# Kernel tuning notes

Hardware: AMD Instinct MI355X
Metric: run time of the kernel (lower is better)

## Reference

```python
import jax, jax.numpy as jnp
import numpy as np

EMBED_DIM = 512
NUM_HEADS = 8
HEAD_DIM = EMBED_DIM // NUM_HEADS
SCALE = HEAD_DIM ** -0.5


def setup_inputs() -> dict:
    key = jax.random.key(0)
    ks = jax.random.split(key, 5)
    B, N, C = 4, 2048, EMBED_DIM
    s = 0.02
    return {
        "x": jax.random.normal(ks[0], (B, N, C), jnp.float32),
        "qkv_w": jax.random.normal(ks[1], (3 * C, C), jnp.float32) * s,
        "qkv_b": jax.random.normal(ks[2], (3 * C,), jnp.float32) * s,
        "proj_w": jax.random.normal(ks[3], (C, C), jnp.float32) * s,
        "proj_b": jax.random.normal(ks[4], (C,), jnp.float32) * s,
    }


def reference(x, qkv_w, qkv_b, proj_w, proj_b):
    B, N, C = x.shape
    H, D = NUM_HEADS, HEAD_DIM
    # qkv: (B, N, 3C) -> (3, B, H, N, D)
    qkv = x @ qkv_w.T + qkv_b
    qkv = qkv.reshape(B, N, 3, H, D).transpose(2, 0, 3, 1, 4)
    q, k, v = qkv[0], qkv[1], qkv[2]
    attn = jnp.einsum("bhnd,bhmd->bhnm", q, k) * SCALE  # (B,H,N,N)
    attn = jax.nn.softmax(attn, axis=-1)
    out = jnp.einsum("bhnm,bhmd->bhnd", attn, v)  # (B,H,N,D)
    out = out.transpose(0, 2, 1, 3).reshape(B, N, C)
    return out @ proj_w.T + proj_b
```

## Files before the change

### kernel.cpp

```cpp
#include <hip/hip_runtime.h>

#define ED 512
#define NH 8
#define HD 64
#define BB 4
#define SEQ 2048
#define MTOT (BB*SEQ)

typedef float f32x4 __attribute__((ext_vector_type(4)));
typedef float f32x16 __attribute__((ext_vector_type(16)));
typedef __bf16 bf16x8 __attribute__((ext_vector_type(8)));
typedef int i32x2 __attribute__((ext_vector_type(2)));
typedef unsigned int u32x4 __attribute__((ext_vector_type(4)));

__device__ __forceinline__ unsigned short f2bf(float f) {
  unsigned int u = __float_as_uint(f);
  u += 0x7FFFu + ((u >> 16) & 1u);
  return (unsigned short)(u >> 16);
}

__device__ __forceinline__ unsigned int cvtpk(float lo, float hi) {
  unsigned int r;
  asm volatile("v_cvt_pk_bf16_f32 %0, %1, %2" : "=v"(r) : "v"(lo), "v"(hi));
  return r;
}

__device__ __forceinline__ void async16(const void* g, void* l) {
  auto gp = (const __attribute__((address_space(1))) unsigned int*)(uintptr_t)(g);
  auto lp = (__attribute__((address_space(3))) unsigned int*)(uintptr_t)(l);
  __builtin_amdgcn_global_load_lds(gp, lp, 16, 0, 0);
}

#define N4_X   1048576
#define N4_WQ  196608
#define N4_WP  65536
__global__ void cvt_all(const float* __restrict__ x,
                        const float* __restrict__ wq_in,
                        const float* __restrict__ wp_in,
                        unsigned short* __restrict__ xb,
                        unsigned short* __restrict__ wq,
                        unsigned short* __restrict__ wp) {
  int i = blockIdx.x * blockDim.x + threadIdx.x;
  const float* src; unsigned short* dst; int off;
  if (i < N4_X)              { src = x;     dst = xb; off = i; }
  else if (i < N4_X + N4_WQ) { src = wq_in; dst = wq; off = i - N4_X; }
  else                       { src = wp_in; dst = wp; off = i - (N4_X + N4_WQ); }
  float4 v = reinterpret_cast<const float4*>(src)[off];
  ushort4 o;
  o.x = f2bf(v.x); o.y = f2bf(v.y); o.z = f2bf(v.z); o.w = f2bf(v.w);
  reinterpret_cast<ushort4*>(dst)[off] = o;
}

template<int MODE, int BM>
__global__ __launch_bounds__(256)
void gemm_bt(const unsigned short* __restrict__ A,
             const unsigned short* __restrict__ B,
             const float* __restrict__ bias,
             int M, int N, int K,
             unsigned short* __restrict__ Qo,
             unsigned short* __restrict__ Ko,
             unsigned short* __restrict__ Vo,
             float* __restrict__ Co) {
  __shared__ __align__(16) unsigned short As[2][BM * 64];
  __shared__ __align__(16) unsigned short Bs[2][128 * 64];
  const int FI = BM / 32;
  const int t = threadIdx.x;
  const int l = t & 63;
  const int w = t >> 6;
  const int lo = l & 15, hi = l >> 4;
  const int wr = w >> 1, wc = w & 1;
  const int m0 = blockIdx.y * BM;
  const int n0 = blockIdx.x * 128;

  f32x4 acc[FI][4] = {};

  auto stage = [&](int buf, int kt) {
    #pragma unroll
    for (int it = 0; it < BM / 32; ++it) {
      int c = it * 256 + t;
      int row = c >> 3, cin = c & 7;
      int sw = cin ^ (row & 7);
      async16(A + (size_t)(m0 + row) * K + kt * 64 + sw * 8, &As[buf][c * 8]);
    }
    #pragma unroll
    for (int it = 0; it < 4; ++it) {
      int c = it * 256 + t;
      int row = c >> 3, cin = c & 7;
      int sw = cin ^ (row & 7);
      async16(B + (size_t)(n0 + row) * K + kt * 64 + sw * 8, &Bs[buf][c * 8]);
    }
  };

  const int nkt = K >> 6;
  stage(0, 0);
  asm volatile("s_waitcnt vmcnt(0)" ::: "memory");
  __syncthreads();

  for (int kt = 0; kt < nkt; ++kt) {
    const int cur = kt & 1;
    if (kt + 1 < nkt) stage(cur ^ 1, kt + 1);

    __builtin_amdgcn_s_setprio(1);
    #pragma unroll
    for (int kk = 0; kk < 2; ++kk) {
      bf16x8 af[FI], bf[4];
      #pragma unroll
      for (int i = 0; i < FI; ++i) {
        int ra = wr * (BM / 2) + i * 16 + lo;
        int ch = (kk * 4 + hi) ^ (lo & 7);
        af[i] = *reinterpret_cast<const bf16x8*>(&As[cur][ra * 64 + ch * 8]);
      }
      #pragma unroll
      for (int j = 0; j < 4; ++j) {
        int rb = wc * 64 + j * 16 + lo;
        int ch = (kk * 4 + hi) ^ (lo & 7);
        bf[j] = *reinterpret_cast<const bf16x8*>(&Bs[cur][rb * 64 + ch * 8]);
      }
      #pragma unroll
      for (int i = 0; i < FI; ++i)
        #pragma unroll
        for (int j = 0; j < 4; ++j)
          acc[i][j] = __builtin_amdgcn_mfma_f32_16x16x32_bf16(af[i], bf[j], acc[i][j], 0, 0, 0);
    }
    __builtin_amdgcn_s_setprio(0);

    asm volatile("s_waitcnt vmcnt(0)" ::: "memory");
    __syncthreads();
  }

  if (MODE == 0) {
    #pragma unroll
    for (int j = 0; j < 4; ++j) {
      int gcol = n0 + wc * 64 + j * 16 + lo;
      float bv = bias[gcol];
      int which = gcol >> 9;
      int h = (gcol >> 6) & 7;
      int d = gcol & 63;
      #pragma unroll
      for (int i = 0; i < FI; ++i) {
        int rbase = m0 + wr * (BM / 2) + i * 16 + hi * 4;
        int b = rbase >> 11;
        size_t bh = (size_t)(b * NH + h);
        if (which == 2) {
          ushort4 pk;
          pk.x = f2bf(acc[i][j][0] + bv);
          pk.y = f2bf(acc[i][j][1] + bv);
          pk.z = f2bf(acc[i][j][2] + bv);
          pk.w = f2bf(acc[i][j][3] + bv);
          int seq = rbase & 2047;
          *reinterpret_cast<ushort4*>(&Vo[(bh * HD + d) * SEQ + seq]) = pk;
        } else {
          #pragma unroll
          for (int e = 0; e < 4; ++e) {
            int seq = (rbase + e) & 2047;
            float v = acc[i][j][e] + bv;
            if (which == 0)
              Qo[(bh * SEQ + seq) * HD + d] = f2bf(v * 0.18033688f);
            else
              Ko[(bh * SEQ + seq) * HD + d] = f2bf(v);
          }
        }
      }
    }
  } else {
    #pragma unroll
    for (int j = 0; j < 4; ++j) {
      int gcol = n0 + wc * 64 + j * 16 + lo;
      float bv = bias[gcol];
      #pragma unroll
      for (int i = 0; i < FI; ++i) {
        int rbase = m0 + wr * (BM / 2) + i * 16 + hi * 4;
        #pragma unroll
        for (int e = 0; e < 4; ++e)
          Co[(size_t)(rbase + e) * N + gcol] = acc[i][j][e] + bv;
      }
    }
  }
}

__global__ __launch_bounds__(512, 4)
void attn_kernel(const unsigned short* __restrict__ Q,
                 const unsigned short* __restrict__ Kk,
                 const unsigned short* __restrict__ Vt,
                 unsigned short* __restrict__ Ao) {
  __shared__ __align__(16) unsigned short Ks[2][2][64 * 64];
  __shared__ __align__(16) unsigned short Vs[2][2][64 * 64];
  const int t = threadIdx.x;
  const int l = t & 63;
  const int wid = t >> 6;
  const int qg = wid & 3;
  const int kvh = wid >> 2;
  const int l31 = l & 31, lh = l >> 5;
  const int bh = blockIdx.y;
  const int q0 = blockIdx.x * 128;
  const int b = bh >> 3, h = bh & 7;

  bf16x8 qf[4];
  #pragma unroll
  for (int ks = 0; ks < 4; ++ks)
    qf[ks] = *reinterpret_cast<const bf16x8*>(
        &Q[((size_t)bh * SEQ + q0 + qg * 32 + l31) * HD + ks * 16 + lh * 8]);

  f32x16 o0 = {}, o1 = {}, osum = {};
  const __bf16 one1 = (__bf16)1.0f;
  const bf16x8 ones = {one1, one1, one1, one1, one1, one1, one1, one1};

  auto stage = [&](int buf, int kt) {
    const int half = t >> 8;
    const int tt = t & 255;
    const int sbase = half * 1024 + kt * 64;
    #pragma unroll
    for (int it = 0; it < 2; ++it) {
      int c = it * 256 + tt;
      int row = c >> 3, cin = c & 7;
      int sw = cin ^ (row & 7);
      async16(&Kk[((size_t)bh * SEQ + sbase + row) * HD + sw * 8],
              &Ks[half][buf][c * 8]);
    }
    #pragma unroll
    for (int it = 0; it < 2; ++it) {
      int c = it * 256 + tt;
      int row = c >> 3, cin = c & 7;
      int sw = cin ^ (row & 7);
      async16(&Vt[((size_t)bh * HD + row) * SEQ + sbase + sw * 8],
              &Vs[half][buf][c * 8]);
    }
  };

  auto tile = [&](int cur, int kt) {
    if (kt + 1 < 16) stage(cur ^ 1, kt + 1);

    #pragma unroll
    for (int kn = 0; kn < 2; ++kn) {
      f32x16 s = {};
      __builtin_amdgcn_s_setprio(1);
      #pragma unroll
      for (int ks = 0; ks < 4; ++ks) {
        int row = kn * 32 + l31;
        int ch = ((ks * 2 + lh) ^ (l31 & 7)) * 8;
        bf16x8 kf = *reinterpret_cast<const bf16x8*>(&Ks[kvh][cur][row * 64 + ch]);
        s = __builtin_amdgcn_mfma_f32_32x32x16_bf16(kf, qf[ks], s, 0, 0, 0);
      }
      __builtin_amdgcn_s_setprio(0);

      #pragma unroll
      for (int i = 0; i < 16; ++i) s[i] = __builtin_amdgcn_exp2f(s[i]);

      #pragma unroll
      for (int hs = 0; hs < 2; ++hs) {
        unsigned int w0 = cvtpk(s[8 * hs + 0], s[8 * hs + 1]);
        unsigned int w1 = cvtpk(s[8 * hs + 2], s[8 * hs + 3]);
        unsigned int w2 = cvtpk(s[8 * hs + 4], s[8 * hs + 5]);
        unsigned int w3 = cvtpk(s[8 * hs + 6], s[8 * hs + 7]);
        i32x2 r0 = __builtin_amdgcn_permlane32_swap((int)w0, (int)w2, false, false);
        i32x2 r1 = __builtin_amdgcn_permlane32_swap((int)w1, (int)w3, false, false);
        u32x4 fw = {(unsigned int)r0.x, (unsigned int)r1.x,
                    (unsigned int)r0.y, (unsigned int)r1.y};
        bf16x8 pf = __builtin_bit_cast(bf16x8, fw);

        int ss = kn * 2 + hs;
        int vch = ((ss * 2 + lh) ^ (l31 & 7)) * 8;
        __builtin_amdgcn_s_setprio(1);
        osum = __builtin_amdgcn_mfma_f32_32x32x16_bf16(pf, ones, osum, 0, 0, 0);
        bf16x8 vf0 = *reinterpret_cast<const bf16x8*>(&Vs[kvh][cur][l31 * 64 + vch]);
        bf16x8 vf1 = *reinterpret_cast<const bf16x8*>(&Vs[kvh][cur][(32 + l31) * 64 + vch]);
        o0 = __builtin_amdgcn_mfma_f32_32x32x16_bf16(pf, vf0, o0, 0, 0, 0);
        o1 = __builtin_amdgcn_mfma_f32_32x32x16_bf16(pf, vf1, o1, 0, 0, 0);
        __builtin_amdgcn_s_setprio(0);
      }
    }

    asm volatile("s_waitcnt vmcnt(0)" ::: "memory");
    __syncthreads();
  };

  stage(0, 0);
  asm volatile("s_waitcnt vmcnt(0)" ::: "memory");
  __syncthreads();

  for (int k2 = 0; k2 < 8; ++k2) {
    tile(0, 2 * k2);
    tile(1, 2 * k2 + 1);
  }

  float* lds = reinterpret_cast<float*>(&Ks[0][0][0]);
  if (kvh == 1) {
    int base = (qg * 64 + l) * 48;
    *reinterpret_cast<f32x16*>(&lds[base])      = o0;
    *reinterpret_cast<f32x16*>(&lds[base + 16]) = o1;
    *reinterpret_cast<f32x16*>(&lds[base + 32]) = osum;
  }
  __syncthreads();
  if (kvh == 0) {
    int base = (qg * 64 + l) * 48;
    o0   += *reinterpret_cast<const f32x16*>(&lds[base]);
    o1   += *reinterpret_cast<const f32x16*>(&lds[base + 16]);
    osum += *reinterpret_cast<const f32x16*>(&lds[base + 32]);

    #pragma unroll
    for (int r = 0; r < 16; ++r) {
      int qoff = (r & 3) + 8 * (r >> 2) + 4 * lh;
      int seq = q0 + qg * 32 + qoff;
      float inv = 1.f / osum[r];
      size_t base2 = ((size_t)b * SEQ + seq) * ED + h * HD;
      Ao[base2 + l31]      = f2bf(o0[r] * inv);
      Ao[base2 + 32 + l31] = f2bf(o1[r] * inv);
    }
  }
}

extern "C" void kernel_launch(void* const* d_in, const int* in_sizes, int n_in,
                              void* d_out, int out_size, void* d_ws, size_t ws_size,
                              hipStream_t stream) {
  const float* x      = (const float*)d_in[0];
  const float* qkv_w  = (const float*)d_in[1];
  const float* qkv_b  = (const float*)d_in[2];
  const float* proj_w = (const float*)d_in[3];
  const float* proj_b = (const float*)d_in[4];
  float* out = (float*)d_out;

  char* ws = (char*)d_ws;
  unsigned short* xb = (unsigned short*)(ws);
  unsigned short* wq = (unsigned short*)(ws + 8388608);
  unsigned short* wp = (unsigned short*)(ws + 9961472);
  unsigned short* Q  = (unsigned short*)(ws + 10485760);
  unsigned short* Kb = (unsigned short*)(ws + 18874368);
  unsigned short* Vt = (unsigned short*)(ws + 27262976);
  unsigned short* Ao = (unsigned short*)(ws + 35651584);

  cvt_all<<<(N4_X + N4_WQ + N4_WP + 255) / 256, 256, 0, stream>>>(
      x, qkv_w, proj_w, xb, wq, wp);

  dim3 g1(12, 128);
  gemm_bt<0, 64><<<g1, 256, 0, stream>>>(xb, wq, qkv_b, MTOT, 3 * ED, ED, Q, Kb, Vt, nullptr);

  dim3 ga(SEQ / 128, BB * NH);
  attn_kernel<<<ga, 512, 0, stream>>>(Q, Kb, Vt, Ao);

  dim3 g2(4, 128);
  gemm_bt<1, 64><<<g2, 256, 0, stream>>>(Ao, wp, proj_b, MTOT, ED, ED, nullptr, nullptr, nullptr, out);
}
```

Measured before the change: 86.88 us.

## Halve attention waves, give each wave two query sub-tiles to reuse K/V fragments

The attention kernel now launches 256 threads per block instead of 512. Each wave processes two 32-row query sub-tiles, so every K and V fragment read from LDS feeds two MFMAs, which halves LDS read traffic per unit of compute. The final cross-KV-half reduction uses a swizzled float4 LDS layout split across the K and V buffers. In exchange, register pressure roughly doubles (six accumulators plus two sets of Q fragments), fewer waves are available to hide latency, and each thread issues twice as many async copies when staging tiles.

```diff
diff --git a/kernel.cpp b/kernel.cpp
--- a/kernel.cpp
+++ b/kernel.cpp
@@ -178,7 +178,7 @@
   }
 }
 
-__global__ __launch_bounds__(512, 4)
+__global__ __launch_bounds__(256, 2)
 void attn_kernel(const unsigned short* __restrict__ Q,
                  const unsigned short* __restrict__ Kk,
                  const unsigned short* __restrict__ Vt,
@@ -188,38 +188,41 @@
   const int t = threadIdx.x;
   const int l = t & 63;
   const int wid = t >> 6;
-  const int qg = wid & 3;
-  const int kvh = wid >> 2;
+  const int qg = wid >> 1;
+  const int kvh = wid & 1;
   const int l31 = l & 31, lh = l >> 5;
   const int bh = blockIdx.y;
   const int q0 = blockIdx.x * 128;
   const int b = bh >> 3, h = bh & 7;
 
-  bf16x8 qf[4];
+  bf16x8 qfA[4], qfB[4];
   #pragma unroll
-  for (int ks = 0; ks < 4; ++ks)
-    qf[ks] = *reinterpret_cast<const bf16x8*>(
-        &Q[((size_t)bh * SEQ + q0 + qg * 32 + l31) * HD + ks * 16 + lh * 8]);
-
-  f32x16 o0 = {}, o1 = {}, osum = {};
+  for (int ks = 0; ks < 4; ++ks) {
+    size_t rowA = (size_t)bh * SEQ + q0 + qg * 64 + l31;
+    qfA[ks] = *reinterpret_cast<const bf16x8*>(&Q[rowA * HD + ks * 16 + lh * 8]);
+    qfB[ks] = *reinterpret_cast<const bf16x8*>(&Q[(rowA + 32) * HD + ks * 16 + lh * 8]);
+  }
+
+  f32x16 oA0 = {}, oA1 = {}, osA = {};
+  f32x16 oB0 = {}, oB1 = {}, osB = {};
   const __bf16 one1 = (__bf16)1.0f;
   const bf16x8 ones = {one1, one1, one1, one1, one1, one1, one1, one1};
 
   auto stage = [&](int buf, int kt) {
-    const int half = t >> 8;
-    const int tt = t & 255;
+    const int half = t >> 7;
+    const int tt = t & 127;
     const int sbase = half * 1024 + kt * 64;
     #pragma unroll
-    for (int it = 0; it < 2; ++it) {
-      int c = it * 256 + tt;
+    for (int it = 0; it < 4; ++it) {
+      int c = it * 128 + tt;
       int row = c >> 3, cin = c & 7;
       int sw = cin ^ (row & 7);
       async16(&Kk[((size_t)bh * SEQ + sbase + row) * HD + sw * 8],
               &Ks[half][buf][c * 8]);
     }
     #pragma unroll
-    for (int it = 0; it < 2; ++it) {
-      int c = it * 256 + tt;
+    for (int it = 0; it < 4; ++it) {
+      int c = it * 128 + tt;
       int row = c >> 3, cin = c & 7;
       int sw = cin ^ (row & 7);
       async16(&Vt[((size_t)bh * HD + row) * SEQ + sbase + sw * 8],
@@ -227,45 +230,57 @@
     }
   };
 
+  auto pack = [&](const f32x16& s, int hs) -> bf16x8 {
+    unsigned int w0 = cvtpk(s[8 * hs + 0], s[8 * hs + 1]);
+    unsigned int w1 = cvtpk(s[8 * hs + 2], s[8 * hs + 3]);
+    unsigned int w2 = cvtpk(s[8 * hs + 4], s[8 * hs + 5]);
+    unsigned int w3 = cvtpk(s[8 * hs + 6], s[8 * hs + 7]);
+    i32x2 r0 = __builtin_amdgcn_permlane32_swap((int)w0, (int)w2, false, false);
+    i32x2 r1 = __builtin_amdgcn_permlane32_swap((int)w1, (int)w3, false, false);
+    u32x4 fw = {(unsigned int)r0.x, (unsigned int)r1.x,
+                (unsigned int)r0.y, (unsigned int)r1.y};
+    return __builtin_bit_cast(bf16x8, fw);
+  };
+
   auto tile = [&](int cur, int kt) {
     if (kt + 1 < 16) stage(cur ^ 1, kt + 1);
 
     #pragma unroll
     for (int kn = 0; kn < 2; ++kn) {
-      f32x16 s = {};
+      f32x16 s0 = {}, s1 = {};
       __builtin_amdgcn_s_setprio(1);
       #pragma unroll
       for (int ks = 0; ks < 4; ++ks) {
         int row = kn * 32 + l31;
         int ch = ((ks * 2 + lh) ^ (l31 & 7)) * 8;
         bf16x8 kf = *reinterpret_cast<const bf16x8*>(&Ks[kvh][cur][row * 64 + ch]);
-        s = __builtin_amdgcn_mfma_f32_32x32x16_bf16(kf, qf[ks], s, 0, 0, 0);
+        s0 = __builtin_amdgcn_mfma_f32_32x32x16_bf16(kf, qfA[ks], s0, 0, 0, 0);
+        s1 = __builtin_amdgcn_mfma_f32_32x32x16_bf16(kf, qfB[ks], s1, 0, 0, 0);
       }
       __builtin_amdgcn_s_setprio(0);
 
       #pragma unroll
-      for (int i = 0; i < 16; ++i) s[i] = __builtin_amdgcn_exp2f(s[i]);
+      for (int i = 0; i < 16; ++i) {
+        s0[i] = __builtin_amdgcn_exp2f(s0[i]);
+        s1[i] = __builtin_amdgcn_exp2f(s1[i]);
+      }
 
       #pragma unroll
       for (int hs = 0; hs < 2; ++hs) {
-        unsigned int w0 = cvtpk(s[8 * hs + 0], s[8 * hs + 1]);
-        unsigned int w1 = cvtpk(s[8 * hs + 2], s[8 * hs + 3]);
-        unsigned int w2 = cvtpk(s[8 * hs + 4], s[8 * hs + 5]);
-        unsigned int w3 = cvtpk(s[8 * hs + 6], s[8 * hs + 7]);
-        i32x2 r0 = __builtin_amdgcn_permlane32_swap((int)w0, (int)w2, false, false);
-        i32x2 r1 = __builtin_amdgcn_permlane32_swap((int)w1, (int)w3, false, false);
-        u32x4 fw = {(unsigned int)r0.x, (unsigned int)r1.x,
-                    (unsigned int)r0.y, (unsigned int)r1.y};
-        bf16x8 pf = __builtin_bit_cast(bf16x8, fw);
+        bf16x8 pfA = pack(s0, hs);
+        bf16x8 pfB = pack(s1, hs);
 
         int ss = kn * 2 + hs;
         int vch = ((ss * 2 + lh) ^ (l31 & 7)) * 8;
-        __builtin_amdgcn_s_setprio(1);
-        osum = __builtin_amdgcn_mfma_f32_32x32x16_bf16(pf, ones, osum, 0, 0, 0);
         bf16x8 vf0 = *reinterpret_cast<const bf16x8*>(&Vs[kvh][cur][l31 * 64 + vch]);
         bf16x8 vf1 = *reinterpret_cast<const bf16x8*>(&Vs[kvh][cur][(32 + l31) * 64 + vch]);
-        o0 = __builtin_amdgcn_mfma_f32_32x32x16_bf16(pf, vf0, o0, 0, 0, 0);
-        o1 = __builtin_amdgcn_mfma_f32_32x32x16_bf16(pf, vf1, o1, 0, 0, 0);
+        __builtin_amdgcn_s_setprio(1);
+        osA = __builtin_amdgcn_mfma_f32_32x32x16_bf16(pfA, ones, osA, 0, 0, 0);
+        oA0 = __builtin_amdgcn_mfma_f32_32x32x16_bf16(pfA, vf0, oA0, 0, 0, 0);
+        oA1 = __builtin_amdgcn_mfma_f32_32x32x16_bf16(pfA, vf1, oA1, 0, 0, 0);
+        osB = __builtin_amdgcn_mfma_f32_32x32x16_bf16(pfB, ones, osB, 0, 0, 0);
+        oB0 = __builtin_amdgcn_mfma_f32_32x32x16_bf16(pfB, vf0, oB0, 0, 0, 0);
+        oB1 = __builtin_amdgcn_mfma_f32_32x32x16_bf16(pfB, vf1, oB1, 0, 0, 0);
         __builtin_amdgcn_s_setprio(0);
       }
     }
@@ -283,28 +298,49 @@
     tile(1, 2 * k2 + 1);
   }
 
-  float* lds = reinterpret_cast<float*>(&Ks[0][0][0]);
+  float* lds = (qg == 0) ? reinterpret_cast<float*>(&Ks[0][0][0])
+                         : reinterpret_cast<float*>(&Vs[0][0][0]);
+  auto coff = [&](int c) { return (size_t)l * 96 + (((c & ~7) | ((c & 7) ^ (l & 7))) << 2); };
   if (kvh == 1) {
-    int base = (qg * 64 + l) * 48;
-    *reinterpret_cast<f32x16*>(&lds[base])      = o0;
-    *reinterpret_cast<f32x16*>(&lds[base + 16]) = o1;
-    *reinterpret_cast<f32x16*>(&lds[base + 32]) = osum;
+    #pragma unroll
+    for (int c = 0; c < 4; ++c) {
+      *reinterpret_cast<f32x4*>(lds + coff(c))      = f32x4{oA0[4*c], oA0[4*c+1], oA0[4*c+2], oA0[4*c+3]};
+      *reinterpret_cast<f32x4*>(lds + coff(c + 4))  = f32x4{oA1[4*c], oA1[4*c+1], oA1[4*c+2], oA1[4*c+3]};
+      *reinterpret_cast<f32x4*>(lds + coff(c + 8))  = f32x4{osA[4*c], osA[4*c+1], osA[4*c+2], osA[4*c+3]};
+      *reinterpret_cast<f32x4*>(lds + coff(c + 12)) = f32x4{oB0[4*c], oB0[4*c+1], oB0[4*c+2], oB0[4*c+3]};
+      *reinterpret_cast<f32x4*>(lds + coff(c + 16)) = f32x4{oB1[4*c], oB1[4*c+1], oB1[4*c+2], oB1[4*c+3]};
+      *reinterpret_cast<f32x4*>(lds + coff(c + 20)) = f32x4{osB[4*c], osB[4*c+1], osB[4*c+2], osB[4*c+3]};
+    }
   }
   __syncthreads();
   if (kvh == 0) {
-    int base = (qg * 64 + l) * 48;
-    o0   += *reinterpret_cast<const f32x16*>(&lds[base]);
-    o1   += *reinterpret_cast<const f32x16*>(&lds[base + 16]);
-    osum += *reinterpret_cast<const f32x16*>(&lds[base + 32]);
+    #pragma unroll
+    for (int c = 0; c < 4; ++c) {
+      f32x4 a0 = *reinterpret_cast<const f32x4*>(lds + coff(c));
+      f32x4 a1 = *reinterpret_cast<const f32x4*>(lds + coff(c + 4));
+      f32x4 a2 = *reinterpret_cast<const f32x4*>(lds + coff(c + 8));
+      f32x4 b0 = *reinterpret_cast<const f32x4*>(lds + coff(c + 12));
+      f32x4 b1 = *reinterpret_cast<const f32x4*>(lds + coff(c + 16));
+      f32x4 b2 = *reinterpret_cast<const f32x4*>(lds + coff(c + 20));
+      #pragma unroll
+      for (int e = 0; e < 4; ++e) {
+        oA0[4*c+e] += a0[e]; oA1[4*c+e] += a1[e]; osA[4*c+e] += a2[e];
+        oB0[4*c+e] += b0[e]; oB1[4*c+e] += b1[e]; osB[4*c+e] += b2[e];
+      }
+    }
 
     #pragma unroll
     for (int r = 0; r < 16; ++r) {
       int qoff = (r & 3) + 8 * (r >> 2) + 4 * lh;
-      int seq = q0 + qg * 32 + qoff;
-      float inv = 1.f / osum[r];
-      size_t base2 = ((size_t)b * SEQ + seq) * ED + h * HD;
-      Ao[base2 + l31]      = f2bf(o0[r] * inv);
-      Ao[base2 + 32 + l31] = f2bf(o1[r] * inv);
+      int seqA = q0 + qg * 64 + qoff;
+      float invA = 1.f / osA[r];
+      size_t baseA = ((size_t)b * SEQ + seqA) * ED + h * HD;
+      Ao[baseA + l31]      = f2bf(oA0[r] * invA);
+      Ao[baseA + 32 + l31] = f2bf(oA1[r] * invA);
+      float invB = 1.f / osB[r];
+      size_t baseB = baseA + (size_t)32 * ED;
+      Ao[baseB + l31]      = f2bf(oB0[r] * invB);
+      Ao[baseB + 32 + l31] = f2bf(oB1[r] * invB);
     }
   }
 }
@@ -335,7 +371,7 @@
   gemm_bt<0, 64><<<g1, 256, 0, stream>>>(xb, wq, qkv_b, MTOT, 3 * ED, ED, Q, Kb, Vt, nullptr);
 
   dim3 ga(SEQ / 128, BB * NH);
-  attn_kernel<<<ga, 512, 0, stream>>>(Q, Kb, Vt, Ao);
+  attn_kernel<<<ga, 256, 0, stream>>>(Q, Kb, Vt, Ao);
 
   dim3 g2(4, 128);
   gemm_bt<1, 64><<<g2, 256, 0, stream>>>(Ao, wp, proj_b, MTOT, ED, ED, nullptr, nullptr, nullptr, out);
```

Measured after the change: 88.39 us. About the same (+1.7%).
